# Performance work log

Hardware: AMD Instinct MI355X
Metric: run time of the kernel (lower is better)

The kernel has to match this reference:

```python
import jax, jax.numpy as jnp
import numpy as np

B, S, D, H = 2, 2048, 1024, 16
HD = D // H
BAND_LOWER, BAND_UPPER = -1, 0  # tf.linalg.band_part args -> causal


def _causal_add_mask(seq_len):
    # 1 - band_part(ones, lower, upper); 1 where attention is DISALLOWED
    i = jnp.arange(seq_len)[:, None]
    j = jnp.arange(seq_len)[None, :]
    keep = jnp.ones((seq_len, seq_len), bool)
    if BAND_LOWER >= 0:
        keep = keep & ((i - j) <= BAND_LOWER)
    if BAND_UPPER >= 0:
        keep = keep & ((j - i) <= BAND_UPPER)
    return 1.0 - keep.astype(jnp.float32)


def setup_inputs() -> dict:
    key = jax.random.key(0)
    ks = jax.random.split(key, 5)
    scale = 1.0 / np.sqrt(D)
    return {
        "x": jax.random.normal(ks[0], (B, S, D), jnp.float32),
        "wq": jax.random.normal(ks[1], (D, D), jnp.float32) * scale,
        "bq": jnp.zeros((D,), jnp.float32),
        "wk": jax.random.normal(ks[2], (D, D), jnp.float32) * scale,
        "bk": jnp.zeros((D,), jnp.float32),
        "wv": jax.random.normal(ks[3], (D, D), jnp.float32) * scale,
        "bv": jnp.zeros((D,), jnp.float32),
        "wo": jax.random.normal(ks[4], (D, D), jnp.float32) * scale,
        "bo": jnp.zeros((D,), jnp.float32),
    }


def _split_heads(t):
    # [B, S, D] -> [B, H, S, HD]
    return t.reshape(B, S, H, HD).transpose(0, 2, 1, 3)


def reference(x, wq, bq, wk, bk, wv, bv, wo, bo):
    q = _split_heads(x @ wq + bq)
    k = _split_heads(x @ wk + bk)
    v = _split_heads(x @ wv + bv)
    mask = _causal_add_mask(S)  # [S, S], 1 where masked
    logits = jnp.einsum("bhqd,bhkd->bhqk", q, k) / jnp.sqrt(
        jnp.asarray(HD, jnp.float32)
    )
    logits = logits + mask * -1e9
    attn = jax.nn.softmax(logits, axis=-1)
    out = jnp.einsum("bhqk,bhkd->bhqd", attn, v)  # [B, H, S, HD]
    out = out.transpose(0, 2, 1, 3).reshape(B, S, D)
    return out @ wo + bo
```

## Files before the change

### kernel.cpp

```cpp
#include <hip/hip_runtime.h>

#define S_  2048
#define D_  1024
#define H_  16
#define HD_ 64
#define M_  4096
#define K_  1024
#define NEL 4194304

typedef short  bf16x8 __attribute__((ext_vector_type(8)));
typedef float  f32x4  __attribute__((ext_vector_type(4)));
typedef float  f32x16 __attribute__((ext_vector_type(16)));
typedef unsigned int   u32;
typedef unsigned int   u32x4v __attribute__((ext_vector_type(4)));
typedef unsigned short u16;
typedef unsigned short u16x4 __attribute__((ext_vector_type(4)));

#define MFMA16(c,a,b) (c) = __builtin_amdgcn_mfma_f32_16x16x32_bf16((a),(b),(c),0,0,0)
#define MFMA32(c,a,b) (c) = __builtin_amdgcn_mfma_f32_32x32x16_bf16((a),(b),(c),0,0,0)

#define QSCALE 0.18033688011112042f

__device__ __forceinline__ u16 f2bf(float f) {
    union { float f; unsigned u; } v; v.f = f;
    unsigned u = v.u;
    u += 0x7FFFu + ((u >> 16) & 1u);
    return (u16)(u >> 16);
}

__device__ __forceinline__ u32 cvtpk(float lo, float hi) {
    u32 r;
    asm("v_cvt_pk_bf16_f32 %0, %1, %2" : "=v"(r) : "v"(lo), "v"(hi));
    return r;
}

__device__ __forceinline__ void gload16(const void* g, void* l) {
    __builtin_amdgcn_global_load_lds(
        (const __attribute__((address_space(1))) unsigned*)g,
        (__attribute__((address_space(3))) unsigned*)l, 16, 0, 0);
}

__global__ __launch_bounds__(256) void cvt_x(const float* __restrict__ x,
                                             u16* __restrict__ xb) {
    const int i = (blockIdx.x * 256 + threadIdx.x) * 8;
    f32x4 a = *(const f32x4*)&x[i];
    f32x4 b = *(const f32x4*)&x[i + 4];
    u16 t[8];
#pragma unroll
    for (int j = 0; j < 4; ++j) { t[j] = f2bf(a[j]); t[4 + j] = f2bf(b[j]); }
    *(bf16x8*)&xb[i] = *(const bf16x8*)t;
}

__global__ __launch_bounds__(256) void cvt_w(const float* __restrict__ w0,
                                             const float* __restrict__ w1,
                                             const float* __restrict__ w2,
                                             const float* __restrict__ w3,
                                             u16* __restrict__ Wt) {
    __shared__ float T[64][65];
    const float* W = blockIdx.z == 0 ? w0 : blockIdx.z == 1 ? w1
                   : blockIdx.z == 2 ? w2 : w3;
    const int k0 = blockIdx.x * 64, n0 = blockIdx.y * 64;
    const int r  = threadIdx.x >> 2, c0 = (threadIdx.x & 3) * 16;
#pragma unroll
    for (int j = 0; j < 4; ++j)
        *(f32x4*)&T[r][c0 + j * 4] = *(const f32x4*)&W[(size_t)(k0 + r) * D_ + n0 + c0 + j * 4];
    __syncthreads();
    u16 tmp[16];
#pragma unroll
    for (int j = 0; j < 16; ++j) tmp[j] = f2bf(T[c0 + j][r]);
    u16* dst = Wt + ((size_t)blockIdx.z * 1024 + n0 + r) * K_ + k0 + c0;
    *(bf16x8*)dst       = *(const bf16x8*)tmp;
    *(bf16x8*)(dst + 8) = *(const bf16x8*)(tmp + 8);
}

template <int BM, int MODE>
__global__ __launch_bounds__(256) void gemm2(
    const u16* __restrict__ A, const u16* __restrict__ Bt,
    const float* __restrict__ b0, const float* __restrict__ b1,
    const float* __restrict__ b2, void* __restrict__ Out)
{
    __shared__ u16 As[BM * 32];
    __shared__ u16 Bs[128 * 32];
    const int tid = threadIdx.x, lane = tid & 63, wid = tid >> 6;
    const int lr = lane & 15, lg = lane >> 4;
    const int n0 = blockIdx.x * 128, m0 = blockIdx.y * BM;
    const int wm = (wid >> 1) * (BM / 2), wn = (wid & 1) * 64;
    const int lrow = lane >> 2, lch = lane & 3;

    f32x4 acc[BM / 32][4] = {};

    for (int k0 = 0; k0 < K_; k0 += 32) {
        __syncthreads();
#pragma unroll
        for (int t = 0; t < BM / 64; ++t) {
            const int row = wid * (BM / 4) + t * 16 + lrow;
            gload16(A + (size_t)(m0 + row) * K_ + k0 + lch * 8,
                    (u16*)As + row * 32 + lch * 8);
        }
#pragma unroll
        for (int t = 0; t < 2; ++t) {
            const int row = wid * 32 + t * 16 + lrow;
            gload16(Bt + (size_t)(n0 + row) * K_ + k0 + lch * 8,
                    (u16*)Bs + row * 32 + lch * 8);
        }
        __syncthreads();

        bf16x8 af[BM / 32], bf[4];
#pragma unroll
        for (int i = 0; i < BM / 32; ++i)
            af[i] = *(const bf16x8*)&As[(wm + i * 16 + lr) * 32 + lg * 8];
#pragma unroll
        for (int j = 0; j < 4; ++j)
            bf[j] = *(const bf16x8*)&Bs[(wn + j * 16 + lr) * 32 + lg * 8];
#pragma unroll
        for (int i = 0; i < BM / 32; ++i)
#pragma unroll
            for (int j = 0; j < 4; ++j) MFMA16(acc[i][j], af[i], bf[j]);
    }

#pragma unroll
    for (int i = 0; i < BM / 32; ++i) {
#pragma unroll
        for (int j = 0; j < 4; ++j) {
            const int n = n0 + wn + j * 16 + lr;
            const int m = m0 + wm + i * 16 + lg * 4;
            if constexpr (MODE == 0) {
                const int which = n >> 10, nn = n & 1023;
                const float* bp = which == 0 ? b0 : which == 1 ? b1 : b2;
                const float bv = bp[nn];
                u16* qkv = (u16*)Out;
                const int h = nn >> 6, hd = nn & 63;
                const int b = m >> 11, s = m & 2047;
                if (which == 2) {
                    u16x4 pk;
#pragma unroll
                    for (int r4 = 0; r4 < 4; ++r4) pk[r4] = f2bf(acc[i][j][r4] + bv);
                    *(u16x4*)&qkv[(size_t)2 * NEL +
                                  ((size_t)(b * H_ + h) * HD_ + hd) * S_ + s] = pk;
                } else {
                    const float sc = (which == 0) ? QSCALE : 1.0f;
                    const size_t bas = (size_t)which * NEL + (size_t)(b * H_ + h) * S_ * HD_;
#pragma unroll
                    for (int r4 = 0; r4 < 4; ++r4)
                        qkv[bas + (size_t)(s + r4) * HD_ + hd] =
                            f2bf((acc[i][j][r4] + bv) * sc);
                }
            } else {
                const float bv = b0[n];
                float* o = (float*)Out;
#pragma unroll
                for (int r4 = 0; r4 < 4; ++r4)
                    o[(size_t)(m + r4) * D_ + n] = acc[i][j][r4] + bv;
            }
        }
    }
}

__global__ __launch_bounds__(256) void attn7(
    const u16* __restrict__ Q, const u16* __restrict__ K,
    const u16* __restrict__ Vt, u16* __restrict__ CTX)
{
    __shared__ float OB[2][64][33];
    __shared__ float MB[2][64], LB[2][64];

    const int tid  = threadIdx.x;
    const int lane = tid & 63, wv = tid >> 6;
    const int lo = lane & 31, hi = lane >> 5;
    const int idx = blockIdx.x;
    const int bh  = idx & 31;
    const int pu  = idx >> 5;
    const size_t base  = (size_t)bh * S_ * HD_;
    const size_t vbase = (size_t)bh * HD_ * S_;
    const int b = bh >> 4, h = bh & 15;

    for (int mem = 0; mem < 2; ++mem) {
        const int qb  = mem == 0 ? 63 - pu : pu;
        const int wq0 = qb * 32;

        bf16x8 qf[4];
#pragma unroll
        for (int ks = 0; ks < 4; ++ks)
            qf[ks] = *(const bf16x8*)&Q[base + (size_t)(wq0 + lo) * HD_ + ks * 16 + hi * 8];

        f32x16 acc[2] = {};
        float m_ = -1e30f, l_ = 0.f;
        const int nt = (wq0 >> 6) + 1;

        for (int t = wv; t < nt; t += 4) {
            const int kv0 = t * 64;
            const bool sub1 = (kv0 + 32 <= wq0 + 31);

            f32x16 cT[2];
#pragma unroll
            for (int i = 0; i < 16; ++i) { cT[0][i] = 0.f; cT[1][i] = 0.f; }
            __builtin_amdgcn_s_setprio(1);
#pragma unroll
            for (int ks = 0; ks < 4; ++ks) {
                bf16x8 kf = *(const bf16x8*)&K[base + (size_t)(kv0 + lo) * HD_ + ks * 16 + hi * 8];
                MFMA32(cT[0], kf, qf[ks]);
            }
            if (sub1) {
#pragma unroll
                for (int ks = 0; ks < 4; ++ks) {
                    bf16x8 kf = *(const bf16x8*)&K[base + (size_t)(kv0 + 32 + lo) * HD_ + ks * 16 + hi * 8];
                    MFMA32(cT[1], kf, qf[ks]);
                }
            }
            __builtin_amdgcn_s_setprio(0);

            bf16x8 vf[2][4];
#pragma unroll
            for (int dt = 0; dt < 2; ++dt)
#pragma unroll
                for (int ks = 0; ks < 4; ++ks)
                    if (ks < 2 || sub1)
                        vf[dt][ks] = *(const bf16x8*)&Vt[vbase + (size_t)(dt * 32 + lo) * S_ +
                                                         kv0 + ks * 16 + hi * 8];

            if (kv0 + 63 > wq0) {
                const int qg = wq0 + lo;
#pragma unroll
                for (int tt = 0; tt < 2; ++tt)
#pragma unroll
                    for (int r = 0; r < 16; ++r) {
                        const int kvg = kv0 + tt * 32 + (r & 3) + 8 * (r >> 2) + 4 * hi;
                        if (kvg > qg) cT[tt][r] = -1e9f;
                    }
            }

            float m8[8];
#pragma unroll
            for (int i = 0; i < 8; ++i)
                m8[i] = fmaxf(fmaxf(cT[0][i], cT[0][i + 8]), fmaxf(cT[1][i], cT[1][i + 8]));
            float mx = fmaxf(fmaxf(fmaxf(m8[0], m8[1]), fmaxf(m8[2], m8[3])),
                             fmaxf(fmaxf(m8[4], m8[5]), fmaxf(m8[6], m8[7])));
            mx = fmaxf(mx, __shfl_xor(mx, 32));

            if (!__all(mx <= m_ + 11.5f)) {
                const float mn = fmaxf(m_, mx);
                const float al = exp2f(m_ - mn);
                m_ = mn; l_ *= al;
                float alr[16];
#pragma unroll
                for (int r = 0; r < 16; ++r)
                    alr[r] = __shfl(al, (r & 3) + 8 * (r >> 2) + 4 * hi);
#pragma unroll
                for (int r = 0; r < 16; ++r) { acc[0][r] *= alr[r]; acc[1][r] *= alr[r]; }
            }

#pragma unroll
            for (int i = 0; i < 16; ++i) {
                cT[0][i] = exp2f(cT[0][i] - m_);
                cT[1][i] = exp2f(cT[1][i] - m_);
            }
            float s8[8];
#pragma unroll
            for (int i = 0; i < 8; ++i)
                s8[i] = (cT[0][i] + cT[0][i + 8]) + (cT[1][i] + cT[1][i + 8]);
            float ssum = ((s8[0] + s8[1]) + (s8[2] + s8[3])) +
                         ((s8[4] + s8[5]) + (s8[6] + s8[7]));
            ssum += __shfl_xor(ssum, 32);
            l_ += ssum;

            u32 pk[2][8];
#pragma unroll
            for (int tt = 0; tt < 2; ++tt)
#pragma unroll
                for (int w = 0; w < 8; ++w)
                    pk[tt][w] = cvtpk(cT[tt][2 * w], cT[tt][2 * w + 1]);

#pragma unroll
            for (int ks = 0; ks < 4; ++ks) {
                if (ks < 2 || sub1) {
                    const int tt = ks >> 1;
                    const int ma = (2 * ks) & 3;
                    const int mb = (2 * ks + 1) & 3;
                    const u32 own0 = hi ? pk[tt][2 * mb]     : pk[tt][2 * ma];
                    const u32 own1 = hi ? pk[tt][2 * mb + 1] : pk[tt][2 * ma + 1];
                    const u32 snd0 = hi ? pk[tt][2 * ma]     : pk[tt][2 * mb];
                    const u32 snd1 = hi ? pk[tt][2 * ma + 1] : pk[tt][2 * mb + 1];
                    const u32 rcv0 = (u32)__shfl_xor((int)snd0, 32);
                    const u32 rcv1 = (u32)__shfl_xor((int)snd1, 32);
                    u32x4v afv;
                    afv.x = hi ? rcv0 : own0;
                    afv.y = hi ? rcv1 : own1;
                    afv.z = hi ? own0 : rcv0;
                    afv.w = hi ? own1 : rcv1;
                    const bf16x8 af = __builtin_bit_cast(bf16x8, afv);
                    __builtin_amdgcn_s_setprio(1);
                    MFMA32(acc[0], af, vf[0][ks]);
                    MFMA32(acc[1], af, vf[1][ks]);
                    __builtin_amdgcn_s_setprio(0);
                }
            }
        }

        if (wv >= 2) {
            const int bb = wv - 2;
#pragma unroll
            for (int r = 0; r < 16; ++r) {
                OB[bb][lane][r]      = acc[0][r];
                OB[bb][lane][16 + r] = acc[1][r];
            }
            MB[bb][lane] = m_;
            LB[bb][lane] = l_;
        }
        __syncthreads();
        if (wv < 2) {
            const int bb = wv;
            const float m1 = MB[bb][lane], l1 = LB[bb][lane];
            const float mM = fmaxf(m_, m1);
            const float a0 = exp2f(m_ - mM), a1 = exp2f(m1 - mM);
            m_ = mM;
            l_ = l_ * a0 + l1 * a1;
            float a0r[16], a1r[16];
#pragma unroll
            for (int r = 0; r < 16; ++r) {
                const int rq = (r & 3) + 8 * (r >> 2) + 4 * hi;
                a0r[r] = __shfl(a0, rq);
                a1r[r] = __shfl(a1, rq);
            }
#pragma unroll
            for (int r = 0; r < 16; ++r) {
                acc[0][r] = acc[0][r] * a0r[r] + OB[bb][lane][r]      * a1r[r];
                acc[1][r] = acc[1][r] * a0r[r] + OB[bb][lane][16 + r] * a1r[r];
            }
        }
        __syncthreads();
        if (wv == 1) {
#pragma unroll
            for (int r = 0; r < 16; ++r) {
                OB[0][lane][r]      = acc[0][r];
                OB[0][lane][16 + r] = acc[1][r];
            }
            MB[0][lane] = m_;
            LB[0][lane] = l_;
        }
        __syncthreads();
        if (wv == 0) {
            const float m1 = MB[0][lane], l1 = LB[0][lane];
            const float mM = fmaxf(m_, m1);
            const float a0 = exp2f(m_ - mM), a1 = exp2f(m1 - mM);
            l_ = l_ * a0 + l1 * a1;
            float a0r[16], a1r[16];
#pragma unroll
            for (int r = 0; r < 16; ++r) {
                const int rq = (r & 3) + 8 * (r >> 2) + 4 * hi;
                a0r[r] = __shfl(a0, rq);
                a1r[r] = __shfl(a1, rq);
            }
#pragma unroll
            for (int r = 0; r < 16; ++r) {
                acc[0][r] = acc[0][r] * a0r[r] + OB[0][lane][r]      * a1r[r];
                acc[1][r] = acc[1][r] * a0r[r] + OB[0][lane][16 + r] * a1r[r];
            }

            const float linv = 1.0f / l_;
            float lrr[16];
#pragma unroll
            for (int r = 0; r < 16; ++r)
                lrr[r] = __shfl(linv, (r & 3) + 8 * (r >> 2) + 4 * hi);
#pragma unroll
            for (int r = 0; r < 16; ++r) {
                const int q = wq0 + (r & 3) + 8 * (r >> 2) + 4 * hi;
                u16* o = &CTX[(size_t)(b * S_ + q) * D_ + h * HD_ + lo];
                o[0]  = f2bf(acc[0][r] * lrr[r]);
                o[32] = f2bf(acc[1][r] * lrr[r]);
            }
        }
        __syncthreads();
    }
}

extern "C" void kernel_launch(void* const* d_in, const int* in_sizes, int n_in,
                              void* d_out, int out_size, void* d_ws, size_t ws_size,
                              hipStream_t stream)
{
    const float* x  = (const float*)d_in[0];
    const float* wq = (const float*)d_in[1];
    const float* bq = (const float*)d_in[2];
    const float* wk = (const float*)d_in[3];
    const float* bk = (const float*)d_in[4];
    const float* wv = (const float*)d_in[5];
    const float* bv = (const float*)d_in[6];
    const float* wo = (const float*)d_in[7];
    const float* bo = (const float*)d_in[8];

    char* ws = (char*)d_ws;
    u16*   xb    = (u16*)ws;
    u16*   WtAll = (u16*)(ws + (size_t)8  * 1024 * 1024);
    u16*   qkv   = (u16*)(ws + (size_t)16 * 1024 * 1024);
    u16*   ctx   = xb;

    cvt_x<<<2048, 256, 0, stream>>>(x, xb);
    cvt_w<<<dim3(16, 16, 4), 256, 0, stream>>>(wq, wk, wv, wo, WtAll);

    gemm2<128, 0><<<dim3(24, 32), 256, 0, stream>>>(xb, WtAll, bq, bk, bv, qkv);

    attn7<<<dim3(1024), 256, 0, stream>>>(qkv, qkv + NEL, qkv + 2 * (size_t)NEL, ctx);

    gemm2<64, 1><<<dim3(8, 64), 256, 0, stream>>>(ctx, WtAll + (size_t)3072 * K_,
                                                  bo, bo, bo, d_out);
}
```

Measured before the change: 159.6 us.

## Process attention KV tiles in 32-row halves to cut register pressure

The attention kernel now walks each 64-key tile as one or two 32-key sub-tiles, keeping a single score accumulator instead of two. V fragments are loaded per sub-tile, after the softmax, rather than all up front, and K/V addresses become incrementing row pointers. A launch-bounds hint asking for 3 blocks per SM is added to steer the register budget toward higher occupancy. In exchange, the online-softmax max/rescale step runs twice per tile, and the loads are issued later, so there is less memory-latency hiding within a wave.

```diff
diff --git a/kernel.cpp b/kernel.cpp
--- a/kernel.cpp
+++ b/kernel.cpp
@@ -156,7 +156,7 @@
     }
 }
 
-__global__ __launch_bounds__(256) void attn7(
+__global__ __launch_bounds__(256, 3) void attn8(
     const u16* __restrict__ Q, const u16* __restrict__ K,
     const u16* __restrict__ Vt, u16* __restrict__ CTX)
 {
@@ -186,113 +186,110 @@
         float m_ = -1e30f, l_ = 0.f;
         const int nt = (wq0 >> 6) + 1;
 
+        const u16* kRow  = K  + base  + (size_t)(wv * 64 + lo) * HD_ + hi * 8;
+        const u16* vRow0 = Vt + vbase + (size_t)lo * S_        + wv * 64 + hi * 8;
+        const u16* vRow1 = Vt + vbase + (size_t)(32 + lo) * S_ + wv * 64 + hi * 8;
+
         for (int t = wv; t < nt; t += 4) {
             const int kv0 = t * 64;
-            const bool sub1 = (kv0 + 32 <= wq0 + 31);
-
-            f32x16 cT[2];
-#pragma unroll
-            for (int i = 0; i < 16; ++i) { cT[0][i] = 0.f; cT[1][i] = 0.f; }
-            __builtin_amdgcn_s_setprio(1);
-#pragma unroll
-            for (int ks = 0; ks < 4; ++ks) {
-                bf16x8 kf = *(const bf16x8*)&K[base + (size_t)(kv0 + lo) * HD_ + ks * 16 + hi * 8];
-                MFMA32(cT[0], kf, qf[ks]);
-            }
-            if (sub1) {
+            const int nsub = (kv0 + 32 <= wq0 + 31) ? 2 : 1;
+
+            for (int sub = 0; sub < nsub; ++sub) {
+                const int so = sub * 32;
+
+                f32x16 cT = {};
+                __builtin_amdgcn_s_setprio(1);
 #pragma unroll
                 for (int ks = 0; ks < 4; ++ks) {
-                    bf16x8 kf = *(const bf16x8*)&K[base + (size_t)(kv0 + 32 + lo) * HD_ + ks * 16 + hi * 8];
-                    MFMA32(cT[1], kf, qf[ks]);
-                }
-            }
-            __builtin_amdgcn_s_setprio(0);
-
-            bf16x8 vf[2][4];
-#pragma unroll
-            for (int dt = 0; dt < 2; ++dt)
-#pragma unroll
-                for (int ks = 0; ks < 4; ++ks)
-                    if (ks < 2 || sub1)
-                        vf[dt][ks] = *(const bf16x8*)&Vt[vbase + (size_t)(dt * 32 + lo) * S_ +
-                                                         kv0 + ks * 16 + hi * 8];
-
-            if (kv0 + 63 > wq0) {
-                const int qg = wq0 + lo;
-#pragma unroll
-                for (int tt = 0; tt < 2; ++tt)
+                    bf16x8 kf = *(const bf16x8*)(kRow + so * HD_ + ks * 16);
+                    MFMA32(cT, kf, qf[ks]);
+                }
+                __builtin_amdgcn_s_setprio(0);
+
+                if (kv0 + so + 31 > wq0) {
+                    const int qg = wq0 + lo;
 #pragma unroll
                     for (int r = 0; r < 16; ++r) {
-                        const int kvg = kv0 + tt * 32 + (r & 3) + 8 * (r >> 2) + 4 * hi;
-                        if (kvg > qg) cT[tt][r] = -1e9f;
+                        const int kvg = kv0 + so + (r & 3) + 8 * (r >> 2) + 4 * hi;
+                        if (kvg > qg) cT[r] = -1e9f;
                     }
-            }
-
-            float m8[8];
-#pragma unroll
-            for (int i = 0; i < 8; ++i)
-                m8[i] = fmaxf(fmaxf(cT[0][i], cT[0][i + 8]), fmaxf(cT[1][i], cT[1][i + 8]));
-            float mx = fmaxf(fmaxf(fmaxf(m8[0], m8[1]), fmaxf(m8[2], m8[3])),
-                             fmaxf(fmaxf(m8[4], m8[5]), fmaxf(m8[6], m8[7])));
-            mx = fmaxf(mx, __shfl_xor(mx, 32));
-
-            if (!__all(mx <= m_ + 11.5f)) {
-                const float mn = fmaxf(m_, mx);
-                const float al = exp2f(m_ - mn);
-                m_ = mn; l_ *= al;
-                float alr[16];
-#pragma unroll
-                for (int r = 0; r < 16; ++r)
-                    alr[r] = __shfl(al, (r & 3) + 8 * (r >> 2) + 4 * hi);
-#pragma unroll
-                for (int r = 0; r < 16; ++r) { acc[0][r] *= alr[r]; acc[1][r] *= alr[r]; }
-            }
-
-#pragma unroll
-            for (int i = 0; i < 16; ++i) {
-                cT[0][i] = exp2f(cT[0][i] - m_);
-                cT[1][i] = exp2f(cT[1][i] - m_);
-            }
-            float s8[8];
-#pragma unroll
-            for (int i = 0; i < 8; ++i)
-                s8[i] = (cT[0][i] + cT[0][i + 8]) + (cT[1][i] + cT[1][i + 8]);
-            float ssum = ((s8[0] + s8[1]) + (s8[2] + s8[3])) +
-                         ((s8[4] + s8[5]) + (s8[6] + s8[7]));
-            ssum += __shfl_xor(ssum, 32);
-            l_ += ssum;
-
-            u32 pk[2][8];
-#pragma unroll
-            for (int tt = 0; tt < 2; ++tt)
+                }
+
+                float t8[8];
+#pragma unroll
+                for (int i = 0; i < 8; ++i) t8[i] = fmaxf(cT[i], cT[i + 8]);
+                float mx = fmaxf(fmaxf(fmaxf(t8[0], t8[1]), fmaxf(t8[2], t8[3])),
+                                 fmaxf(fmaxf(t8[4], t8[5]), fmaxf(t8[6], t8[7])));
+                mx = fmaxf(mx, __shfl_xor(mx, 32));
+
+                if (!__all(mx <= m_ + 11.5f)) {
+                    const float mn = fmaxf(m_, mx);
+                    const float al = exp2f(m_ - mn);
+                    m_ = mn; l_ *= al;
+                    float alr[16];
+#pragma unroll
+                    for (int r = 0; r < 16; ++r)
+                        alr[r] = __shfl(al, (r & 3) + 8 * (r >> 2) + 4 * hi);
+#pragma unroll
+                    for (int r = 0; r < 16; ++r) { acc[0][r] *= alr[r]; acc[1][r] *= alr[r]; }
+                }
+
+#pragma unroll
+                for (int i = 0; i < 16; ++i) cT[i] = exp2f(cT[i] - m_);
+#pragma unroll
+                for (int i = 0; i < 8; ++i) t8[i] = cT[i] + cT[i + 8];
+                float ssum = ((t8[0] + t8[1]) + (t8[2] + t8[3])) +
+                             ((t8[4] + t8[5]) + (t8[6] + t8[7]));
+                ssum += __shfl_xor(ssum, 32);
+                l_ += ssum;
+
+                u32 pk[8];
 #pragma unroll
                 for (int w = 0; w < 8; ++w)
-                    pk[tt][w] = cvtpk(cT[tt][2 * w], cT[tt][2 * w + 1]);
-
-#pragma unroll
-            for (int ks = 0; ks < 4; ++ks) {
-                if (ks < 2 || sub1) {
-                    const int tt = ks >> 1;
-                    const int ma = (2 * ks) & 3;
-                    const int mb = (2 * ks + 1) & 3;
-                    const u32 own0 = hi ? pk[tt][2 * mb]     : pk[tt][2 * ma];
-                    const u32 own1 = hi ? pk[tt][2 * mb + 1] : pk[tt][2 * ma + 1];
-                    const u32 snd0 = hi ? pk[tt][2 * ma]     : pk[tt][2 * mb];
-                    const u32 snd1 = hi ? pk[tt][2 * ma + 1] : pk[tt][2 * mb + 1];
+                    pk[w] = cvtpk(cT[2 * w], cT[2 * w + 1]);
+
+                bf16x8 vf00 = *(const bf16x8*)(vRow0 + so);
+                bf16x8 vf10 = *(const bf16x8*)(vRow1 + so);
+                bf16x8 vf01 = *(const bf16x8*)(vRow0 + so + 16);
+                bf16x8 vf11 = *(const bf16x8*)(vRow1 + so + 16);
+
+                bf16x8 af0, af1;
+                {
+                    const u32 own0 = hi ? pk[2] : pk[0];
+                    const u32 own1 = hi ? pk[3] : pk[1];
+                    const u32 snd0 = hi ? pk[0] : pk[2];
+                    const u32 snd1 = hi ? pk[1] : pk[3];
                     const u32 rcv0 = (u32)__shfl_xor((int)snd0, 32);
                     const u32 rcv1 = (u32)__shfl_xor((int)snd1, 32);
-                    u32x4v afv;
-                    afv.x = hi ? rcv0 : own0;
-                    afv.y = hi ? rcv1 : own1;
-                    afv.z = hi ? own0 : rcv0;
-                    afv.w = hi ? own1 : rcv1;
-                    const bf16x8 af = __builtin_bit_cast(bf16x8, afv);
-                    __builtin_amdgcn_s_setprio(1);
-                    MFMA32(acc[0], af, vf[0][ks]);
-                    MFMA32(acc[1], af, vf[1][ks]);
-                    __builtin_amdgcn_s_setprio(0);
-                }
-            }
+                    u32x4v v;
+                    v.x = hi ? rcv0 : own0;  v.y = hi ? rcv1 : own1;
+                    v.z = hi ? own0 : rcv0;  v.w = hi ? own1 : rcv1;
+                    af0 = __builtin_bit_cast(bf16x8, v);
+                }
+                {
+                    const u32 own0 = hi ? pk[6] : pk[4];
+                    const u32 own1 = hi ? pk[7] : pk[5];
+                    const u32 snd0 = hi ? pk[4] : pk[6];
+                    const u32 snd1 = hi ? pk[5] : pk[7];
+                    const u32 rcv0 = (u32)__shfl_xor((int)snd0, 32);
+                    const u32 rcv1 = (u32)__shfl_xor((int)snd1, 32);
+                    u32x4v v;
+                    v.x = hi ? rcv0 : own0;  v.y = hi ? rcv1 : own1;
+                    v.z = hi ? own0 : rcv0;  v.w = hi ? own1 : rcv1;
+                    af1 = __builtin_bit_cast(bf16x8, v);
+                }
+
+                __builtin_amdgcn_s_setprio(1);
+                MFMA32(acc[0], af0, vf00);
+                MFMA32(acc[1], af0, vf10);
+                MFMA32(acc[0], af1, vf01);
+                MFMA32(acc[1], af1, vf11);
+                __builtin_amdgcn_s_setprio(0);
+            }
+
+            kRow  += 256 * HD_;
+            vRow0 += 256;
+            vRow1 += 256;
         }
 
         if (wv >= 2) {
@@ -397,7 +394,7 @@
 
     gemm2<128, 0><<<dim3(24, 32), 256, 0, stream>>>(xb, WtAll, bq, bk, bv, qkv);
 
-    attn7<<<dim3(1024), 256, 0, stream>>>(qkv, qkv + NEL, qkv + 2 * (size_t)NEL, ctx);
+    attn8<<<dim3(1024), 256, 0, stream>>>(qkv, qkv + NEL, qkv + 2 * (size_t)NEL, ctx);
 
     gemm2<64, 1><<<dim3(8, 64), 256, 0, stream>>>(ctx, WtAll + (size_t)3072 * K_,
                                                   bo, bo, bo, d_out);
```

After: 172.6 us. 8.2% more time.
